# Kernel tuning notes

Hardware: AMD Instinct MI355X
Metric: run time of the kernel (lower is better)

## Reference

```python
import jax, jax.numpy as jnp
import numpy as np

B, S, E, F, N = 2, 1024, 1024, 2048, 8


def setup_inputs() -> dict:
    key = jax.random.key(0)
    k0, k1, k2, k3, k4 = jax.random.split(key, 5)
    x = jax.random.normal(k0, (B, S, E), dtype=jnp.float32)
    # fan_in-scaled params, matching nd_dense_init(1.0, 'fan_in', ...)
    gate_kernel = jax.random.normal(k1, (E, N), dtype=jnp.float32) / np.sqrt(E).astype(np.float32)
    w0 = jax.random.normal(k2, (N, E, F), dtype=jnp.float32) / np.sqrt(E).astype(np.float32)
    w1 = jax.random.normal(k3, (N, E, F), dtype=jnp.float32) / np.sqrt(E).astype(np.float32)
    wo = jax.random.normal(k4, (N, F, E), dtype=jnp.float32) / np.sqrt(F).astype(np.float32)
    return {"x": x, "gate_kernel": gate_kernel, "w0": w0, "w1": w1, "wo": wo, "top_k": 2}


def reference(x, gate_kernel, w0, w1, wo, top_k):
    # x: [B, S, E] -> tokens [T, E]
    b, s, e = x.shape
    n = gate_kernel.shape[-1]
    xf = x.reshape(b * s, e)
    # Router: gate logits + top-k expert selection, softmax over top-k (fp32, as in permute())
    logits = jnp.einsum('te,en->tn', xf, gate_kernel)
    top_w, top_e = jax.lax.top_k(logits, top_k)               # [T, K]
    probs = jax.nn.softmax(top_w.astype(jnp.float32), axis=-1)  # [T, K]
    # Combine weights per (token, expert): scatter top-k probs into [T, N]
    combine = jnp.einsum('tk,tkn->tn', probs, jax.nn.one_hot(top_e, n, dtype=jnp.float32))
    # Expert FFN (dropless): h = silu(x@w0) * (x@w1); out_e = h @ wo   (same math as gmm path)
    h0 = jnp.einsum('te,nef->ntf', xf, w0)                    # [N, T, F]
    h1 = jnp.einsum('te,nef->ntf', xf, w1)
    h = jax.nn.silu(h0) * h1
    expert_out = jnp.einsum('ntf,nfe->nte', h, wo)            # [N, T, E]
    # Weighted combine over experts (matches unpermute's 'BKE,BK->BE' in fp32)
    out = jnp.einsum('nte,tn->te', expert_out, combine)
    return out.reshape(b, s, e)
```

## Files before the change

### kernel.cpp

```cpp
#include <hip/hip_runtime.h>
#include <hip/hip_bf16.h>

#define T_TOK 2048
#define E_DIM 1024
#define F_DIM 2048
#define N_EXP 8

typedef __attribute__((ext_vector_type(8))) short short8;
typedef __attribute__((ext_vector_type(4))) float f32x4;

__device__ __forceinline__ short bf2s(__hip_bfloat16 v) {
  union { __hip_bfloat16 b; short s; } u; u.b = v; return u.s;
}

__device__ __forceinline__ void gload_lds16(const void* g, void* l) {
  __builtin_amdgcn_global_load_lds((const __attribute__((address_space(1))) void*)g,
                                   (__attribute__((address_space(3))) void*)l, 16, 0, 0);
}

__device__ __forceinline__ void transpose_tile(const float* __restrict__ src,
                                               __hip_bfloat16* __restrict__ dst,
                                               int C, int R, int r0, int c0,
                                               int tid, short* lds) {
  int u = tid >> 3, o = tid & 7;
#pragma unroll
  for (int it = 0; it < 2; ++it) {
    int r = it * 32 + u;
    const float* p = src + (size_t)(r0 + r) * C + c0 + o * 8;
    float4 v0 = *(const float4*)p;
    float4 v1 = *(const float4*)(p + 4);
    float vv[8] = {v0.x, v0.y, v0.z, v0.w, v1.x, v1.y, v1.z, v1.w};
#pragma unroll
    for (int j = 0; j < 8; ++j) {
      int c = o * 8 + j;
      int rho = (c + (c >> 3)) & 7;
      lds[c * 64 + ((r + 8 * rho) & 63)] = bf2s(__float2bfloat16(vv[j]));
    }
  }
  __syncthreads();
#pragma unroll
  for (int it = 0; it < 2; ++it) {
    int c = it * 32 + u;
    int rho = (c + (c >> 3)) & 7;
    int b = (o + rho) & 7;
    short8 q = *(const short8*)&lds[c * 64 + b * 8];
    *(short8*)(dst + (size_t)(c0 + c) * R + r0 + o * 8) = q;
  }
}

__global__ __launch_bounds__(256) void prep_kernel(const float* __restrict__ w0,
                                                   const float* __restrict__ w1,
                                                   const float* __restrict__ x,
                                                   const float* __restrict__ gk,
                                                   __hip_bfloat16* __restrict__ w0t,
                                                   __hip_bfloat16* __restrict__ w1t,
                                                   __hip_bfloat16* __restrict__ xb,
                                                   int* __restrict__ tk_e,
                                                   float* __restrict__ tk_p,
                                                   int* __restrict__ counts) {
  __shared__ short tl[64 * 64];
  int bid = blockIdx.x;
  if (bid < 8192) {
    int which = bid >> 12;
    int tile = bid & 4095;
    int e = tile >> 9;
    int t2 = tile & 511;
    int r0 = (t2 & 15) * 64;
    int c0 = (t2 >> 4) * 64;
    const float* src = (which ? w1 : w0) + (size_t)e * E_DIM * F_DIM;
    __hip_bfloat16* dst = (which ? w1t : w0t) + (size_t)e * E_DIM * F_DIM;
    transpose_tile(src, dst, F_DIM, E_DIM, r0, c0, threadIdx.x, tl);
    return;
  }
  if (bid < 8192 + 1024) {
    size_t i = ((size_t)(bid - 8192) * 256 + threadIdx.x) * 8;
    float4 a = *(const float4*)(x + i);
    float4 b = *(const float4*)(x + i + 4);
    short8 oo;
    oo[0] = bf2s(__float2bfloat16(a.x)); oo[1] = bf2s(__float2bfloat16(a.y));
    oo[2] = bf2s(__float2bfloat16(a.z)); oo[3] = bf2s(__float2bfloat16(a.w));
    oo[4] = bf2s(__float2bfloat16(b.x)); oo[5] = bf2s(__float2bfloat16(b.y));
    oo[6] = bf2s(__float2bfloat16(b.z)); oo[7] = bf2s(__float2bfloat16(b.w));
    *(short8*)(xb + i) = oo;
    return;
  }
  int w = threadIdx.x >> 6, l = threadIdx.x & 63;
  int t = (bid - 9216) * 4 + w;
  const float* xr = x + (size_t)t * E_DIM;
  double acc[N_EXP];
#pragma unroll
  for (int n = 0; n < N_EXP; n++) acc[n] = 0.0;
  for (int j = 0; j < 16; j++) {
    int i = j * 64 + l;
    double xv = (double)xr[i];
    const float* g = gk + (size_t)i * N_EXP;
#pragma unroll
    for (int n = 0; n < N_EXP; n++) acc[n] += xv * (double)g[n];
  }
#pragma unroll
  for (int off = 32; off > 0; off >>= 1) {
#pragma unroll
    for (int n = 0; n < N_EXP; n++) acc[n] += __shfl_down(acc[n], off);
  }
  if (l == 0) {
    int e1 = 0; double v1 = acc[0];
    for (int n = 1; n < N_EXP; n++) if (acc[n] > v1) { v1 = acc[n]; e1 = n; }
    int e2 = -1; double v2 = -1e300;
    for (int n = 0; n < N_EXP; n++) if (n != e1 && acc[n] > v2) { v2 = acc[n]; e2 = n; }
    float ex = __expf((float)(v2 - v1));
    float p1 = 1.f / (1.f + ex);
    float p2 = ex / (1.f + ex);
    tk_e[t * 2 + 0] = e1; tk_p[t * 2 + 0] = p1;
    tk_e[t * 2 + 1] = e2; tk_p[t * 2 + 1] = p2;
    atomicAdd(&counts[e1], 1);
    atomicAdd(&counts[e2], 1);
  }
}

__global__ __launch_bounds__(256) void scanperm_kernel(const int* __restrict__ tk_e,
                                                       const float* __restrict__ tk_p,
                                                       int* __restrict__ ctrl,
                                                       int* __restrict__ slot_tok,
                                                       float* __restrict__ slot_prob,
                                                       int* __restrict__ inv) {
  __shared__ int offs[8], cur[8];
  int tid = threadIdx.x;
  if (tid == 0) {
    int off = 0, idx = 0;
    for (int e = 0; e < N_EXP; e++) {
      offs[e] = off; cur[e] = 0;
      int c = ctrl[e];
      for (int m0 = 0; m0 < c; m0 += 128) {
        ctrl[32 + idx] = e;
        ctrl[96 + idx] = off + m0;
        ctrl[160 + idx] = (c - m0 < 128) ? (c - m0) : 128;
        idx++;
      }
      off += c;
    }
    ctrl[24] = idx;
  }
  __syncthreads();
  for (int g = tid; g < 2 * T_TOK; g += 256) {
    int e = tk_e[g];
    float p = tk_p[g];
    int pos = atomicAdd(&cur[e], 1);
    int slot = offs[e] + pos;
    slot_tok[slot] = g >> 1;
    slot_prob[slot] = p;
    inv[g] = slot;
  }
}

__global__ __launch_bounds__(512, 4) void gemm1_kernel(const __hip_bfloat16* __restrict__ xb,
                                                       const __hip_bfloat16* __restrict__ w0t,
                                                       const __hip_bfloat16* __restrict__ w1t,
                                                       const int* __restrict__ ctrl,
                                                       const int* __restrict__ slot_tok,
                                                       __hip_bfloat16* __restrict__ h,
                                                       const float* __restrict__ wo,
                                                       __hip_bfloat16* __restrict__ wot) {
  __shared__ alignas(16) short lA[128 * 64];
  __shared__ alignas(16) short lB0[128 * 64];
  __shared__ alignas(16) short lB1[128 * 64];

  if (blockIdx.x >= 640) {
    int half = threadIdx.x >> 8, tt = threadIdx.x & 255;
    int tile = (blockIdx.x - 640) * 2 + half;
    int e = tile >> 9;
    int t2 = tile & 511;
    int r0 = (t2 & 31) * 64;
    int c0 = (t2 >> 5) * 64;
    short* tl = half ? (short*)lB0 : (short*)lA;
    transpose_tile(wo + (size_t)e * F_DIM * E_DIM, wot + (size_t)e * E_DIM * F_DIM,
                   E_DIM, F_DIM, r0, c0, tt, tl);
    return;
  }

  int lin = blockIdx.x;
  int logical = (lin & 7) * 80 + (lin >> 3);
  int mt = logical % 40;
  int fy = logical / 40;
  if (mt >= ctrl[24]) return;
  int e = ctrl[32 + mt];
  int slot0 = ctrl[96 + mt];
  int rowsv = ctrl[160 + mt];
  int f0 = fy * 128;

  int tid = threadIdx.x;
  int w = tid >> 6, l = tid & 63;
  int wm = w >> 2, wn = w & 3;
  int frow = l & 15, fk = l >> 4;

  int r1 = tid >> 3;
  int kc = ((tid & 7) ^ (r1 & 7)) * 8;
  int tokA1 = slot_tok[slot0 + r1];
  int tokA2 = slot_tok[slot0 + r1 + 64];
  const __hip_bfloat16* aS1 = xb + (size_t)tokA1 * E_DIM + kc;
  const __hip_bfloat16* aS2 = xb + (size_t)tokA2 * E_DIM + kc;
  const __hip_bfloat16* b0S1 = w0t + ((size_t)e * F_DIM + f0 + r1) * E_DIM + kc;
  const __hip_bfloat16* b0S2 = b0S1 + (size_t)64 * E_DIM;
  const __hip_bfloat16* b1S1 = w1t + ((size_t)e * F_DIM + f0 + r1) * E_DIM + kc;
  const __hip_bfloat16* b1S2 = b1S1 + (size_t)64 * E_DIM;

  f32x4 zero4 = {0.f, 0.f, 0.f, 0.f};
  f32x4 acc0[4][2], acc1[4][2];
#pragma unroll
  for (int mi = 0; mi < 4; mi++)
#pragma unroll
    for (int ni = 0; ni < 2; ni++) { acc0[mi][ni] = zero4; acc1[mi][ni] = zero4; }

  auto stage = [&](int t) {
    int k0 = t * 64;
    gload_lds16(aS1 + k0,  &lA[w * 512]);
    gload_lds16(aS2 + k0,  &lA[4096 + w * 512]);
    gload_lds16(b0S1 + k0, &lB0[w * 512]);
    gload_lds16(b0S2 + k0, &lB0[4096 + w * 512]);
    gload_lds16(b1S1 + k0, &lB1[w * 512]);
    gload_lds16(b1S2 + k0, &lB1[4096 + w * 512]);
  };

  const int NT = E_DIM / 64;
  for (int t = 0; t < NT; ++t) {
    if (t) __syncthreads();
    stage(t);
    __syncthreads();
    __builtin_amdgcn_s_setprio(1);
#pragma unroll
    for (int ks = 0; ks < 2; ++ks) {
      short8 a[4], b0[2], b1[2];
#pragma unroll
      for (int mi = 0; mi < 4; ++mi) {
        int r = wm * 64 + mi * 16 + frow;
        a[mi] = *(const short8*)&lA[r * 64 + ((ks * 4 + fk) ^ (r & 7)) * 8];
      }
#pragma unroll
      for (int ni = 0; ni < 2; ++ni) {
        int n = wn * 32 + ni * 16 + frow;
        int off = n * 64 + ((ks * 4 + fk) ^ (n & 7)) * 8;
        b0[ni] = *(const short8*)&lB0[off];
        b1[ni] = *(const short8*)&lB1[off];
      }
#pragma unroll
      for (int mi = 0; mi < 4; ++mi)
#pragma unroll
        for (int ni = 0; ni < 2; ++ni) {
          acc0[mi][ni] = __builtin_amdgcn_mfma_f32_16x16x32_bf16(a[mi], b0[ni], acc0[mi][ni], 0, 0, 0);
          acc1[mi][ni] = __builtin_amdgcn_mfma_f32_16x16x32_bf16(a[mi], b1[ni], acc1[mi][ni], 0, 0, 0);
        }
    }
    __builtin_amdgcn_s_setprio(0);
  }

#pragma unroll
  for (int mi = 0; mi < 4; ++mi) {
#pragma unroll
    for (int j = 0; j < 4; ++j) {
      int r = wm * 64 + mi * 16 + fk * 4 + j;
      if (r < rowsv) {
        __hip_bfloat16* hr = h + (size_t)(slot0 + r) * F_DIM + f0 + wn * 32;
#pragma unroll
        for (int ni = 0; ni < 2; ++ni) {
          float v0 = acc0[mi][ni][j];
          float v1 = acc1[mi][ni][j];
          float s = (v0 / (1.f + __expf(-v0))) * v1;
          hr[ni * 16 + frow] = __float2bfloat16(s);
        }
      }
    }
  }
}

__global__ __launch_bounds__(512, 4) void gemm2_kernel(const __hip_bfloat16* __restrict__ h,
                                                       const __hip_bfloat16* __restrict__ wot,
                                                       const int* __restrict__ ctrl,
                                                       const float* __restrict__ slot_prob,
                                                       float* __restrict__ parts) {
  int lin = blockIdx.x;
  int logical = (lin & 7) * 40 + (lin >> 3);
  int mt = logical % 40;
  int ey = logical / 40;
  if (mt >= ctrl[24]) return;
  int e = ctrl[32 + mt];
  int slot0 = ctrl[96 + mt];
  int rowsv = ctrl[160 + mt];
  int e0 = ey * 128;

  __shared__ alignas(16) short lA[128 * 64];
  __shared__ alignas(16) short lB[128 * 64];

  int tid = threadIdx.x;
  int w = tid >> 6, l = tid & 63;
  int wm = w >> 2, wn = w & 3;
  int frow = l & 15, fk = l >> 4;

  int r1 = tid >> 3;
  int kc = ((tid & 7) ^ (r1 & 7)) * 8;
  const __hip_bfloat16* aS1 = h + (size_t)(slot0 + r1) * F_DIM + kc;
  const __hip_bfloat16* aS2 = aS1 + (size_t)64 * F_DIM;
  const __hip_bfloat16* bS1 = wot + ((size_t)e * E_DIM + e0 + r1) * F_DIM + kc;
  const __hip_bfloat16* bS2 = bS1 + (size_t)64 * F_DIM;

  f32x4 zero4 = {0.f, 0.f, 0.f, 0.f};
  f32x4 acc[4][2];
#pragma unroll
  for (int mi = 0; mi < 4; mi++)
#pragma unroll
    for (int ni = 0; ni < 2; ni++) acc[mi][ni] = zero4;

  auto stage = [&](int t) {
    int k0 = t * 64;
    gload_lds16(aS1 + k0, &lA[w * 512]);
    gload_lds16(aS2 + k0, &lA[4096 + w * 512]);
    gload_lds16(bS1 + k0, &lB[w * 512]);
    gload_lds16(bS2 + k0, &lB[4096 + w * 512]);
  };

  const int NT = F_DIM / 64;
  for (int t = 0; t < NT; ++t) {
    if (t) __syncthreads();
    stage(t);
    __syncthreads();
    __builtin_amdgcn_s_setprio(1);
#pragma unroll
    for (int ks = 0; ks < 2; ++ks) {
      short8 a[4], b[2];
#pragma unroll
      for (int mi = 0; mi < 4; ++mi) {
        int r = wm * 64 + mi * 16 + frow;
        a[mi] = *(const short8*)&lA[r * 64 + ((ks * 4 + fk) ^ (r & 7)) * 8];
      }
#pragma unroll
      for (int ni = 0; ni < 2; ++ni) {
        int n = wn * 32 + ni * 16 + frow;
        b[ni] = *(const short8*)&lB[n * 64 + ((ks * 4 + fk) ^ (n & 7)) * 8];
      }
#pragma unroll
      for (int mi = 0; mi < 4; ++mi)
#pragma unroll
        for (int ni = 0; ni < 2; ++ni)
          acc[mi][ni] = __builtin_amdgcn_mfma_f32_16x16x32_bf16(a[mi], b[ni], acc[mi][ni], 0, 0, 0);
    }
    __builtin_amdgcn_s_setprio(0);
  }

#pragma unroll
  for (int mi = 0; mi < 4; ++mi) {
#pragma unroll
    for (int j = 0; j < 4; ++j) {
      int r = wm * 64 + mi * 16 + fk * 4 + j;
      if (r < rowsv) {
        int slot = slot0 + r;
        float p = slot_prob[slot];
        float* pr = parts + (size_t)slot * E_DIM + e0 + wn * 32;
#pragma unroll
        for (int ni = 0; ni < 2; ++ni)
          pr[ni * 16 + frow] = p * acc[mi][ni][j];
      }
    }
  }
}

__global__ __launch_bounds__(256) void combine_kernel(const float* __restrict__ parts,
                                                      const int* __restrict__ inv,
                                                      float* __restrict__ out) {
  int g = blockIdx.x * 256 + threadIdx.x;
  int row = g >> 7, c = (g & 127) * 8;
  int s1 = inv[row * 2], s2 = inv[row * 2 + 1];
  const float4* p1 = (const float4*)(parts + (size_t)s1 * E_DIM + c);
  const float4* p2 = (const float4*)(parts + (size_t)s2 * E_DIM + c);
  float4 a0 = p1[0], a1 = p1[1], b0 = p2[0], b1 = p2[1];
  float4 o0 = {a0.x + b0.x, a0.y + b0.y, a0.z + b0.z, a0.w + b0.w};
  float4 o1 = {a1.x + b1.x, a1.y + b1.y, a1.z + b1.z, a1.w + b1.w};
  float4* op = (float4*)(out + (size_t)row * E_DIM + c);
  op[0] = o0; op[1] = o1;
}

extern "C" void kernel_launch(void* const* d_in, const int* in_sizes, int n_in,
                              void* d_out, int out_size, void* d_ws, size_t ws_size,
                              hipStream_t stream) {
  const float* x  = (const float*)d_in[0];
  const float* gk = (const float*)d_in[1];
  const float* w0 = (const float*)d_in[2];
  const float* w1 = (const float*)d_in[3];
  const float* wo = (const float*)d_in[4];
  float* out = (float*)d_out;
  char* ws = (char*)d_ws;

  const size_t SLOTS = 2 * T_TOK + 128;
  const size_t OFF_XB   = 0;
  const size_t OFF_W0T  = OFF_XB  + (size_t)T_TOK * E_DIM * 2;
  const size_t OFF_W1T  = OFF_W0T + (size_t)N_EXP * E_DIM * F_DIM * 2;
  const size_t OFF_WOT  = OFF_W1T + (size_t)N_EXP * E_DIM * F_DIM * 2;
  const size_t OFF_H    = OFF_WOT + (size_t)N_EXP * F_DIM * E_DIM * 2;
  const size_t OFF_STOK = OFF_H   + SLOTS * F_DIM * 2;
  const size_t OFF_SPRB = OFF_STOK + SLOTS * 4;
  const size_t OFF_TKE  = OFF_SPRB + SLOTS * 4;
  const size_t OFF_TKP  = OFF_TKE + (size_t)2 * T_TOK * 4;
  const size_t OFF_INV  = OFF_TKP + (size_t)2 * T_TOK * 4;
  const size_t OFF_CTRL = OFF_INV + (size_t)2 * T_TOK * 4;
  const size_t NEED     = OFF_CTRL + 1024;
  if (ws_size < NEED) return;

  __hip_bfloat16* xb   = (__hip_bfloat16*)(ws + OFF_XB);
  __hip_bfloat16* w0t  = (__hip_bfloat16*)(ws + OFF_W0T);
  __hip_bfloat16* w1t  = (__hip_bfloat16*)(ws + OFF_W1T);
  __hip_bfloat16* wot  = (__hip_bfloat16*)(ws + OFF_WOT);
  __hip_bfloat16* hbuf = (__hip_bfloat16*)(ws + OFF_H);
  float* parts     = (float*)(ws + OFF_W0T);
  int*   slot_tok  = (int*)(ws + OFF_STOK);
  float* slot_prob = (float*)(ws + OFF_SPRB);
  int*   tk_e      = (int*)(ws + OFF_TKE);
  float* tk_p      = (float*)(ws + OFF_TKP);
  int*   inv       = (int*)(ws + OFF_INV);
  int*   ctrl      = (int*)(ws + OFF_CTRL);

  hipMemsetAsync(ctrl, 0, 1024, stream);
  hipMemsetAsync(slot_tok + 2 * T_TOK, 0, 128 * 4, stream);

  prep_kernel<<<9728, 256, 0, stream>>>(w0, w1, x, gk, w0t, w1t, xb, tk_e, tk_p, ctrl);
  scanperm_kernel<<<1, 256, 0, stream>>>(tk_e, tk_p, ctrl, slot_tok, slot_prob, inv);
  gemm1_kernel<<<2688, 512, 0, stream>>>(xb, w0t, w1t, ctrl, slot_tok, hbuf, wo, wot);
  gemm2_kernel<<<320, 512, 0, stream>>>(hbuf, wot, ctrl, slot_prob, parts);
  combine_kernel<<<(T_TOK * 128) / 256, 256, 0, stream>>>(parts, inv, out);
}
```

Baseline: 217.8 us.

## Replace LDS-based weight transposes with register transposes over larger strips

The fp32-to-bf16 weight transposes for w0/w1 (in prep) and wo (in gemm1 tail blocks) no longer stage through shared memory. Each thread now loads an 8x4 register tile and writes 8-element bf16 columns directly, and each block handles a much larger strip with interleaved loads and stores. The x conversion blocks likewise do four chunks each. The goal is to cut LDS traffic, barriers and block-launch overhead on these bandwidth-bound passes. The cost is narrower 16-byte scattered global stores and more registers per thread.

```diff
diff --git a/kernel.cpp b/kernel.cpp
--- a/kernel.cpp
+++ b/kernel.cpp
@@ -18,33 +18,28 @@
                                    (__attribute__((address_space(3))) void*)l, 16, 0, 0);
 }
 
-__device__ __forceinline__ void transpose_tile(const float* __restrict__ src,
-                                               __hip_bfloat16* __restrict__ dst,
-                                               int C, int R, int r0, int c0,
-                                               int tid, short* lds) {
-  int u = tid >> 3, o = tid & 7;
-#pragma unroll
-  for (int it = 0; it < 2; ++it) {
-    int r = it * 32 + u;
-    const float* p = src + (size_t)(r0 + r) * C + c0 + o * 8;
-    float4 v0 = *(const float4*)p;
-    float4 v1 = *(const float4*)(p + 4);
-    float vv[8] = {v0.x, v0.y, v0.z, v0.w, v1.x, v1.y, v1.z, v1.w};
-#pragma unroll
-    for (int j = 0; j < 8; ++j) {
-      int c = o * 8 + j;
-      int rho = (c + (c >> 3)) & 7;
-      lds[c * 64 + ((r + 8 * rho) & 63)] = bf2s(__float2bfloat16(vv[j]));
-    }
-  }
-  __syncthreads();
-#pragma unroll
-  for (int it = 0; it < 2; ++it) {
-    int c = it * 32 + u;
-    int rho = (c + (c >> 3)) & 7;
-    int b = (o + rho) & 7;
-    short8 q = *(const short8*)&lds[c * 64 + b * 8];
-    *(short8*)(dst + (size_t)(c0 + c) * R + r0 + o * 8) = q;
+__device__ __forceinline__ void tr_load(const float* __restrict__ src, int C,
+                                        int r0, int c0, int tid, float4* v) {
+  int l = tid & 63, w = tid >> 6;
+  int r = r0 + 32 * w + 8 * (l >> 4);
+  int c = c0 + 4 * (l & 15);
+  const float* p = src + (size_t)r * C + c;
+#pragma unroll
+  for (int i = 0; i < 8; ++i) v[i] = *(const float4*)(p + (size_t)i * C);
+}
+
+__device__ __forceinline__ void tr_store(__hip_bfloat16* __restrict__ dst, int R,
+                                         int r0, int c0, int tid, const float4* v) {
+  int l = tid & 63, w = tid >> 6;
+  int r = r0 + 32 * w + 8 * (l >> 4);
+  int c = c0 + 4 * (l & 15);
+#pragma unroll
+  for (int j = 0; j < 4; ++j) {
+    short8 q;
+#pragma unroll
+    for (int i = 0; i < 8; ++i)
+      q[i] = bf2s(__float2bfloat16(((const float*)&v[i])[j]));
+    *(short8*)(dst + (size_t)(c + j) * R + r) = q;
   }
 }
 
@@ -58,34 +53,46 @@
                                                    int* __restrict__ tk_e,
                                                    float* __restrict__ tk_p,
                                                    int* __restrict__ counts) {
-  __shared__ short tl[64 * 64];
   int bid = blockIdx.x;
-  if (bid < 8192) {
-    int which = bid >> 12;
-    int tile = bid & 4095;
-    int e = tile >> 9;
-    int t2 = tile & 511;
-    int r0 = (t2 & 15) * 64;
-    int c0 = (t2 >> 4) * 64;
+  if (bid < 1024) {
+    int which = bid >> 9;
+    int bb = bid & 511;
+    int strip = bb >> 1, rhalf = bb & 1;
+    int e = strip >> 5, cs = strip & 31;
+    int c0 = cs * 64;
+    int r0 = rhalf * 512;
     const float* src = (which ? w1 : w0) + (size_t)e * E_DIM * F_DIM;
     __hip_bfloat16* dst = (which ? w1t : w0t) + (size_t)e * E_DIM * F_DIM;
-    transpose_tile(src, dst, F_DIM, E_DIM, r0, c0, threadIdx.x, tl);
+    int tid = threadIdx.x;
+    float4 v0[8], v1[8], v2[8], v3[8];
+    tr_load(src, F_DIM, r0 + 0 * 128, c0, tid, v0);
+    tr_load(src, F_DIM, r0 + 1 * 128, c0, tid, v1);
+    tr_store(dst, E_DIM, r0 + 0 * 128, c0, tid, v0);
+    tr_load(src, F_DIM, r0 + 2 * 128, c0, tid, v2);
+    tr_store(dst, E_DIM, r0 + 1 * 128, c0, tid, v1);
+    tr_load(src, F_DIM, r0 + 3 * 128, c0, tid, v3);
+    tr_store(dst, E_DIM, r0 + 2 * 128, c0, tid, v2);
+    tr_store(dst, E_DIM, r0 + 3 * 128, c0, tid, v3);
     return;
   }
-  if (bid < 8192 + 1024) {
-    size_t i = ((size_t)(bid - 8192) * 256 + threadIdx.x) * 8;
-    float4 a = *(const float4*)(x + i);
-    float4 b = *(const float4*)(x + i + 4);
-    short8 oo;
-    oo[0] = bf2s(__float2bfloat16(a.x)); oo[1] = bf2s(__float2bfloat16(a.y));
-    oo[2] = bf2s(__float2bfloat16(a.z)); oo[3] = bf2s(__float2bfloat16(a.w));
-    oo[4] = bf2s(__float2bfloat16(b.x)); oo[5] = bf2s(__float2bfloat16(b.y));
-    oo[6] = bf2s(__float2bfloat16(b.z)); oo[7] = bf2s(__float2bfloat16(b.w));
-    *(short8*)(xb + i) = oo;
+  if (bid < 1280) {
+    int idx = bid - 1024;
+#pragma unroll
+    for (int j = 0; j < 4; ++j) {
+      size_t i = ((size_t)(idx + j * 256) * 256 + threadIdx.x) * 8;
+      float4 a = *(const float4*)(x + i);
+      float4 b = *(const float4*)(x + i + 4);
+      short8 oo;
+      oo[0] = bf2s(__float2bfloat16(a.x)); oo[1] = bf2s(__float2bfloat16(a.y));
+      oo[2] = bf2s(__float2bfloat16(a.z)); oo[3] = bf2s(__float2bfloat16(a.w));
+      oo[4] = bf2s(__float2bfloat16(b.x)); oo[5] = bf2s(__float2bfloat16(b.y));
+      oo[6] = bf2s(__float2bfloat16(b.z)); oo[7] = bf2s(__float2bfloat16(b.w));
+      *(short8*)(xb + i) = oo;
+    }
     return;
   }
   int w = threadIdx.x >> 6, l = threadIdx.x & 63;
-  int t = (bid - 9216) * 4 + w;
+  int t = (bid - 1280) * 4 + w;
   const float* xr = x + (size_t)t * E_DIM;
   double acc[N_EXP];
 #pragma unroll
@@ -166,14 +173,18 @@
 
   if (blockIdx.x >= 640) {
     int half = threadIdx.x >> 8, tt = threadIdx.x & 255;
-    int tile = (blockIdx.x - 640) * 2 + half;
-    int e = tile >> 9;
-    int t2 = tile & 511;
-    int r0 = (t2 & 31) * 64;
-    int c0 = (t2 >> 5) * 64;
-    short* tl = half ? (short*)lB0 : (short*)lA;
-    transpose_tile(wo + (size_t)e * F_DIM * E_DIM, wot + (size_t)e * E_DIM * F_DIM,
-                   E_DIM, F_DIM, r0, c0, tt, tl);
+    int base = blockIdx.x - 640;
+    int strip = base >> 2, quarter = base & 3;
+    int e = strip >> 4, cs = strip & 15;
+    int c0 = cs * 64;
+    int r0 = quarter * 512 + half * 256;
+    const float* src = wo + (size_t)e * F_DIM * E_DIM;
+    __hip_bfloat16* dst = wot + (size_t)e * E_DIM * F_DIM;
+    float4 va[8], vb[8];
+    tr_load(src, E_DIM, r0, c0, tt, va);
+    tr_load(src, E_DIM, r0 + 128, c0, tt, vb);
+    tr_store(dst, F_DIM, r0, c0, tt, va);
+    tr_store(dst, F_DIM, r0 + 128, c0, tt, vb);
     return;
   }
 
@@ -418,9 +429,9 @@
   hipMemsetAsync(ctrl, 0, 1024, stream);
   hipMemsetAsync(slot_tok + 2 * T_TOK, 0, 128 * 4, stream);
 
-  prep_kernel<<<9728, 256, 0, stream>>>(w0, w1, x, gk, w0t, w1t, xb, tk_e, tk_p, ctrl);
+  prep_kernel<<<1792, 256, 0, stream>>>(w0, w1, x, gk, w0t, w1t, xb, tk_e, tk_p, ctrl);
   scanperm_kernel<<<1, 256, 0, stream>>>(tk_e, tk_p, ctrl, slot_tok, slot_prob, inv);
-  gemm1_kernel<<<2688, 512, 0, stream>>>(xb, w0t, w1t, ctrl, slot_tok, hbuf, wo, wot);
+  gemm1_kernel<<<1152, 512, 0, stream>>>(xb, w0t, w1t, ctrl, slot_tok, hbuf, wo, wot);
   gemm2_kernel<<<320, 512, 0, stream>>>(hbuf, wot, ctrl, slot_prob, parts);
   combine_kernel<<<(T_TOK * 128) / 256, 256, 0, stream>>>(parts, inv, out);
 }
```

Result: no change. 220.2 us (+1.1%).
